# Kernel optimization log

Measured on AMD Instinct MI355X. Metric: run time of the kernel, lower is better.

Reference implementation:

```python
import jax, jax.numpy as jnp
import numpy as np

B, H, W, C, NH, K = 4, 56, 56, 128, 4, 7


def setup_inputs() -> dict:
    key = jax.random.key(0)
    ks = jax.random.split(key, 6)
    x = jax.random.normal(ks[0], (B, H, W, C), dtype=jnp.float32)
    w_qkv = jax.random.normal(ks[1], (C, 3 * C), dtype=jnp.float32) * 0.02
    b_qkv = jnp.zeros((3 * C,), dtype=jnp.float32)
    rpb = jax.random.normal(ks[2], (NH, 2 * K - 1, 2 * K - 1), dtype=jnp.float32) * 0.02
    w_proj = jax.random.normal(ks[3], (C, C), dtype=jnp.float32) * 0.02
    b_proj = jnp.zeros((C,), dtype=jnp.float32)
    return {"x": x, "w_qkv": w_qkv, "b_qkv": b_qkv, "rpb": rpb,
            "w_proj": w_proj, "b_proj": b_proj}


def reference(x, w_qkv, b_qkv, rpb, w_proj, b_proj):
    B_, H_, W_, C_ = x.shape
    nh = rpb.shape[0]
    k = (rpb.shape[1] + 1) // 2          # kernel_size
    hd = C_ // nh                        # head_dim
    nb = k // 2                          # neighborhood radius
    scale = hd ** -0.5

    qkv = (x @ w_qkv + b_qkv).reshape(B_, H_, W_, 3, nh, hd)
    q = qkv[:, :, :, 0].transpose(0, 3, 1, 2, 4) * scale   # [B,nh,H,W,hd]
    kk = qkv[:, :, :, 1].transpose(0, 3, 1, 2, 4)          # [B,nh,H,W,hd]
    v = qkv[:, :, :, 2].transpose(0, 3, 1, 2, 4)           # [B,nh,H,W,hd]

    # NATTEN window start indices: window clamped to stay in-bounds (query shifts off-center at edges)
    si = jnp.clip(jnp.arange(H_) - nb, 0, H_ - k)          # [H]
    sj = jnp.clip(jnp.arange(W_) - nb, 0, W_ - k)          # [W]
    idx_i = si[:, None] + jnp.arange(k)                    # [H,k] absolute key rows
    idx_j = sj[:, None] + jnp.arange(k)                    # [W,k] absolute key cols

    # gather neighborhood keys/values: [B,nh,H,k,W,k,hd] (axes: b n i p j q d)
    k_win = kk[:, :, idx_i][:, :, :, :, idx_j]
    v_win = v[:, :, idx_i][:, :, :, :, idx_j]

    # relative position bias: index = key_pos - query_pos + (k-1)
    rel_i = idx_i - jnp.arange(H_)[:, None] + (k - 1)      # [H,k]
    rel_j = idx_j - jnp.arange(W_)[:, None] + (k - 1)      # [W,k]
    bias = rpb[:, rel_i][:, :, :, rel_j]                   # [nh,H,k,W,k]
    bias = bias.transpose(0, 1, 3, 2, 4)                   # [nh,H,W,k,k]

    attn = jnp.einsum('bnijd,bnipjqd->bnijpq', q, k_win) + bias[None]
    attn = jax.nn.softmax(attn.reshape(B_, nh, H_, W_, k * k), axis=-1)
    attn = attn.reshape(B_, nh, H_, W_, k, k)

    out = jnp.einsum('bnijpq,bnipjqd->bnijd', attn, v_win)  # [B,nh,H,W,hd]
    out = out.transpose(0, 2, 3, 1, 4).reshape(B_, H_, W_, C_)
    return out @ w_proj + b_proj
```

## Files before the change

kernel.cpp:

```cpp
#include <hip/hip_runtime.h>

#define BATCH 4
#define HH 56
#define WW 56
#define CC 128
#define NHD 4
#define HD 32
#define KS 7
#define NB 3
#define HWSZ (HH * WW)
#define RPBW 13
#define QKV_N 384
#define QKV_ELE ((size_t)BATCH * NHD * HWSZ * HD)

typedef unsigned short u16;
typedef unsigned int   u32;
typedef short bf16x8 __attribute__((ext_vector_type(8)));
typedef short bf16x4 __attribute__((ext_vector_type(4)));
typedef float f32x4  __attribute__((ext_vector_type(4)));

static __device__ __forceinline__ u32 f2bf(float f) {
    u32 u = __float_as_uint(f);
    return (u + 0x7FFFu + ((u >> 16) & 1u)) >> 16;
}
static __device__ __forceinline__ float bf2f(u32 h) { return __uint_as_float(h << 16); }

static __device__ __forceinline__ u32 cvtpk(float lo, float hi) {
    u32 d;
    asm("v_cvt_pk_bf16_f32 %0, %1, %2" : "=v"(d) : "v"(lo), "v"(hi));
    return d;
}
static __device__ __forceinline__ void split2(float a, float b, u32& h, u32& l) {
    h = cvtpk(a, b);
    l = cvtpk(a - __uint_as_float(h << 16), b - __uint_as_float(h & 0xffff0000u));
}

#if __has_builtin(__builtin_amdgcn_mfma_f32_16x16x16bf16_1k)
#define MFMA16(a, b, c) __builtin_amdgcn_mfma_f32_16x16x16bf16_1k(a, b, c, 0, 0, 0)
#else
static __device__ __forceinline__ f32x4 mfma16_asm(bf16x4 a, bf16x4 b, f32x4 c) {
    asm("v_mfma_f32_16x16x16_bf16 %0, %1, %2, %0" : "+v"(c) : "v"(a), "v"(b));
    return c;
}
#define MFMA16(a, b, c) mfma16_asm(a, b, c)
#endif

__global__ __launch_bounds__(256) void prep_w(
    const float* __restrict__ w_qkv, const float* __restrict__ w_proj,
    u16* __restrict__ wqT_h, u16* __restrict__ wqT_l,
    u16* __restrict__ wpT_h, u16* __restrict__ wpT_l)
{
    const int e = blockIdx.x * 256 + threadIdx.x;
    float v; u16 *dh, *dl; int idx;
    if (e < 384 * 128) {
        const int n = e >> 7, k = e & 127;
        v = w_qkv[k * QKV_N + n];
        dh = wqT_h; dl = wqT_l; idx = e;
    } else {
        const int e2 = e - 384 * 128;
        const int n = e2 >> 7, k = e2 & 127;
        v = w_proj[k * CC + n];
        dh = wpT_h; dl = wpT_l; idx = e2;
    }
    const u32 h = f2bf(v);
    dh[idx] = (u16)h;
    dl[idx] = (u16)f2bf(v - bf2f(h));
}

#define LP 72

__global__ __launch_bounds__(256) void qkv_mfma(
    const float* __restrict__ x, const u16* __restrict__ wT_h,
    const u16* __restrict__ wT_l, const float* __restrict__ bias,
    float* __restrict__ qb, float* __restrict__ kb, float* __restrict__ vb)
{
    __shared__ __align__(16) u16 Ah[64 * LP], Al[64 * LP];
    __shared__ __align__(16) u16 Bh[128 * LP], Bl[128 * LP];

    const int tid  = threadIdx.x;
    const int lane = tid & 63;
    const int w    = tid >> 6;
    const int wr = w >> 1, wc = w & 1;
    const int lr = lane >> 4, lc = lane & 15;
    const int m0 = blockIdx.x * 64;
    const int tz = blockIdx.y;

    f32x4 acc[2][4];
    #pragma unroll
    for (int nt = 0; nt < 4; ++nt) {
        const float bn = bias[tz * 128 + wc * 64 + nt * 16 + lc];
        acc[0][nt] = (f32x4){bn, bn, bn, bn};
        acc[1][nt] = acc[0][nt];
    }

    for (int kc = 0; kc < 128; kc += 64) {
        #pragma unroll
        for (int it = 0; it < 4; ++it) {
            const int task = tid + it * 256;
            const int row = task >> 4, q4 = task & 15;
            const float4 xv = *(const float4*)(x + (size_t)(m0 + row) * CC + kc + 4 * q4);
            u32 h0, l0, h1, l1;
            split2(xv.x, xv.y, h0, l0);
            split2(xv.z, xv.w, h1, l1);
            const int off = row * LP + 4 * q4;
            *(uint2*)&Ah[off] = make_uint2(h0, h1);
            *(uint2*)&Al[off] = make_uint2(l0, l1);
        }
        #pragma unroll
        for (int it = 0; it < 8; ++it) {
            const int task = tid + it * 256;
            const int hl = task >> 10;
            const int t2 = task & 1023;
            const int n = t2 >> 3, q8 = t2 & 7;
            const u16* src = (hl ? wT_l : wT_h) + (size_t)(tz * 128 + n) * CC + kc + 8 * q8;
            const uint4 vv = *(const uint4*)src;
            u16* dst = (hl ? Bl : Bh) + n * LP + 8 * q8;
            *(uint4*)dst = vv;
        }
        __syncthreads();
        #pragma unroll
        for (int s = 0; s < 2; ++s) {
            const int ko = 32 * s + 8 * lr;
            bf16x8 bfh[4], bfl[4];
            #pragma unroll
            for (int nt = 0; nt < 4; ++nt) {
                const int bo = (wc * 64 + nt * 16 + lc) * LP + ko;
                bfh[nt] = *(const bf16x8*)&Bh[bo];
                bfl[nt] = *(const bf16x8*)&Bl[bo];
            }
            #pragma unroll
            for (int mt = 0; mt < 2; ++mt) {
                const int ao = (wr * 32 + mt * 16 + lc) * LP + ko;
                const bf16x8 afh = *(const bf16x8*)&Ah[ao];
                const bf16x8 afl = *(const bf16x8*)&Al[ao];
                #pragma unroll
                for (int nt = 0; nt < 4; ++nt) {
                    acc[mt][nt] = __builtin_amdgcn_mfma_f32_16x16x32_bf16(afh, bfh[nt], acc[mt][nt], 0, 0, 0);
                    acc[mt][nt] = __builtin_amdgcn_mfma_f32_16x16x32_bf16(afh, bfl[nt], acc[mt][nt], 0, 0, 0);
                    acc[mt][nt] = __builtin_amdgcn_mfma_f32_16x16x32_bf16(afl, bfh[nt], acc[mt][nt], 0, 0, 0);
                }
            }
        }
        __syncthreads();
    }

    const int tzz = tz;
    float* dst      = (tzz == 0) ? qb : (tzz == 1) ? kb : vb;
    const float scl = (tzz == 0) ? 0.17677669529663687f : 1.0f;
    const int b = m0 / HWSZ;
    #pragma unroll
    for (int mt = 0; mt < 2; ++mt) {
        #pragma unroll
        for (int nt = 0; nt < 4; ++nt) {
            const int n = wc * 64 + nt * 16 + lc;
            const int head = n >> 5, d = n & 31;
            #pragma unroll
            for (int r = 0; r < 4; ++r) {
                const int m  = m0 + wr * 32 + mt * 16 + lr * 4 + r;
                const int ij = m - b * HWSZ;
                dst[((size_t)(b * NHD + head) * HWSZ + ij) * HD + d] = acc[mt][nt][r] * scl;
            }
        }
    }
}

__global__ __launch_bounds__(256) void natten_attn(
    const float* __restrict__ qb, const float* __restrict__ kb,
    const float* __restrict__ vb, const float* __restrict__ rpb,
    float* __restrict__ ob)
{
    __shared__ __align__(16) u16 KhS[208 * 32];
    __shared__ __align__(16) u16 KlS[208 * 32];
    __shared__ __align__(16) u16 VhS[26 * 16 * 20];
    __shared__ __align__(16) u16 VlS[26 * 16 * 20];
    __shared__ float rpbs[RPBW * RPBW];

    const int tid  = threadIdx.x;
    const int lane = tid & 63;
    const int wv   = tid >> 6;
    const int g    = lane >> 4;
    const int cl   = lane & 15;

    const int ti = blockIdx.x / 7;
    const int tj = blockIdx.x % 7;
    const int head = blockIdx.y;
    const int b    = blockIdx.z;
    const int R0 = min(max(ti * 8 - NB, 0), HH - 14);
    const int C0 = min(max(tj * 8 - NB, 0), WW - 14);
    const size_t base = (size_t)(b * NHD + head) * HWSZ;

    const int qlq = 16 * wv + cl;
    const int qi  = ti * 8 + (qlq >> 3);
    const int qj  = tj * 8 + (qlq & 7);
    const float* qp = qb + (base + (size_t)qi * WW + qj) * HD + 8 * g;
    const float4 qv0 = *(const float4*)qp;
    const float4 qv1 = *(const float4*)(qp + 4);

    union U8 { u32 u[4]; bf16x8 v; };
    U8 uqh, uql;
    split2(qv0.x, qv0.y, uqh.u[0], uql.u[0]);
    split2(qv0.z, qv0.w, uqh.u[1], uql.u[1]);
    split2(qv1.x, qv1.y, uqh.u[2], uql.u[2]);
    split2(qv1.z, qv1.w, uqh.u[3], uql.u[3]);
    const bf16x8 Qh = uqh.v;
    const bf16x8 Ql = uql.v;

    if (tid < RPBW * RPBW) rpbs[tid] = rpb[head * (RPBW * RPBW) + tid];

    for (int idx = tid; idx < 1568; idx += 256) {
        const int pos = idx >> 3, c4 = idx & 7;
        const int ri = (pos * 293) >> 12;
        const int rj = pos - ri * 14;
        const float4 kv = *(const float4*)(kb + (base + (size_t)(R0 + ri) * WW + (C0 + rj)) * HD + 4 * c4);
        u32 h0, l0, h1, l1;
        split2(kv.x, kv.y, h0, l0);
        split2(kv.z, kv.w, h1, l1);
        *(uint2*)&KhS[pos * 32 + 4 * c4] = make_uint2(h0, h1);
        *(uint2*)&KlS[pos * 32 + 4 * c4] = make_uint2(l0, l1);
    }
    for (int idx = tid; idx < 784; idx += 256) {
        const int pr = idx >> 3, c4 = idx & 7;
        const int pos0 = 2 * pr;
        const int ri0 = (pos0 * 293) >> 12;       const int rj0 = pos0 - ri0 * 14;
        const int ri1 = ((pos0 + 1) * 293) >> 12; const int rj1 = pos0 + 1 - ri1 * 14;
        const float4 va = *(const float4*)(vb + (base + (size_t)(R0 + ri0) * WW + (C0 + rj0)) * HD + 4 * c4);
        const float4 vc = *(const float4*)(vb + (base + (size_t)(R0 + ri1) * WW + (C0 + rj1)) * HD + 4 * c4);
        const int t = pos0 >> 4, kk = pos0 & 15;
        const float a0[4] = {va.x, va.y, va.z, va.w};
        const float a1[4] = {vc.x, vc.y, vc.z, vc.w};
        #pragma unroll
        for (int i = 0; i < 4; ++i) {
            const int d = 4 * c4 + i;
            const int nt = d >> 4, cd = d & 15;
            u32 hh, ll;
            split2(a0[i], a1[i], hh, ll);
            const int off = ((nt * 13 + t) * 16 + cd) * 20 + kk;
            *(u32*)&VhS[off] = hh;
            *(u32*)&VlS[off] = ll;
        }
    }
    for (int idx = tid; idx < 384; idx += 256) {
        const int kp = idx % 6;
        int r = idx / 6;
        const int cd = r & 15; r >>= 4;
        const int nt = r & 1;  const int arr = r >> 1;
        u16* dst = arr ? VlS : VhS;
        *(u32*)&dst[((nt * 13 + 12) * 16 + cd) * 20 + 4 + 2 * kp] = 0u;
    }
    __syncthreads();

    const int qi0  = ti * 8 + 2 * wv;
    const int s_lo = min(max(qi0 - NB, 0), HH - KS);
    const int t0   = min(((s_lo - R0) * 14) >> 4, 5);

    f32x4 p[8];
    #pragma unroll
    for (int tt = 0; tt < 8; ++tt) p[tt] = (f32x4){0.f, 0.f, 0.f, 0.f};
    #pragma unroll
    for (int tt = 0; tt < 8; ++tt) {
        const int ro = (16 * (t0 + tt) + cl) * 32 + 8 * g;
        const bf16x8 kh = *(const bf16x8*)&KhS[ro];
        const bf16x8 kl = *(const bf16x8*)&KlS[ro];
        p[tt] = __builtin_amdgcn_mfma_f32_16x16x32_bf16(kh, Qh, p[tt], 0, 0, 0);
        p[tt] = __builtin_amdgcn_mfma_f32_16x16x32_bf16(kh, Ql, p[tt], 0, 0, 0);
        p[tt] = __builtin_amdgcn_mfma_f32_16x16x32_bf16(kl, Qh, p[tt], 0, 0, 0);
    }

    const int si = min(max(qi - NB, 0), HH - KS);
    const int sj = min(max(qj - NB, 0), WW - KS);
    const int r_si = si - R0, c_sj = sj - C0;
    const int aq = qi - R0, bq = qj - C0;

    float mmax = -3.0e38f;
    #pragma unroll
    for (int tt = 0; tt < 8; ++tt) {
        #pragma unroll
        for (int r = 0; r < 4; ++r) {
            const int pp = 16 * (t0 + tt) + 4 * g + r;
            const int rowp = (pp * 293) >> 12;
            const int colp = pp - rowp * 14;
            const bool ok = (pp < 196) && ((u32)(rowp - r_si) <= 6u) && ((u32)(colp - c_sj) <= 6u);
            int bidx = (rowp - aq + 6) * RPBW + (colp - bq + 6);
            bidx = ok ? bidx : 0;
            const float sv = ok ? (p[tt][r] + rpbs[bidx]) : -3.0e38f;
            p[tt][r] = sv;
            mmax = fmaxf(mmax, sv);
        }
    }
    mmax = fmaxf(mmax, __shfl_xor(mmax, 16, 64));
    mmax = fmaxf(mmax, __shfl_xor(mmax, 32, 64));

    float lsum = 0.f;
    #pragma unroll
    for (int tt = 0; tt < 8; ++tt) {
        #pragma unroll
        for (int r = 0; r < 4; ++r) {
            const float e = __expf(p[tt][r] - mmax);
            p[tt][r] = e;
            lsum += e;
        }
    }
    lsum += __shfl_xor(lsum, 16, 64);
    lsum += __shfl_xor(lsum, 32, 64);
    const float inv = 1.f / lsum;

    bf16x4 pah[8], pal[8];
    #pragma unroll
    for (int tt = 0; tt < 8; ++tt) {
        const float p0 = p[tt][0] * inv, p1 = p[tt][1] * inv;
        const float p2 = p[tt][2] * inv, p3 = p[tt][3] * inv;
        union U4 { u32 u[2]; bf16x4 v; } ua, ub;
        split2(p0, p1, ua.u[0], ub.u[0]);
        split2(p2, p3, ua.u[1], ub.u[1]);
        pah[tt] = ua.v;
        pal[tt] = ub.v;
    }

    f32x4 o[2];
    o[0] = (f32x4){0.f, 0.f, 0.f, 0.f};
    o[1] = (f32x4){0.f, 0.f, 0.f, 0.f};
    #pragma unroll
    for (int tt = 0; tt < 8; ++tt) {
        const int t = t0 + tt;
        #pragma unroll
        for (int nt = 0; nt < 2; ++nt) {
            const int off = ((nt * 13 + t) * 16 + cl) * 20 + 4 * g;
            const bf16x4 vh = *(const bf16x4*)&VhS[off];
            const bf16x4 vl = *(const bf16x4*)&VlS[off];
            o[nt] = MFMA16(pah[tt], vh, o[nt]);
            o[nt] = MFMA16(pal[tt], vh, o[nt]);
            o[nt] = MFMA16(pah[tt], vl, o[nt]);
        }
    }

    #pragma unroll
    for (int nt = 0; nt < 2; ++nt) {
        #pragma unroll
        for (int r = 0; r < 4; ++r) {
            const int qlo = 16 * wv + 4 * g + r;
            const int oqi = ti * 8 + (qlo >> 3);
            const int oqj = tj * 8 + (qlo & 7);
            ob[((size_t)b * HWSZ + (size_t)oqi * WW + oqj) * CC + head * HD + 16 * nt + cl] = o[nt][r];
        }
    }
}

__global__ __launch_bounds__(256) void proj_mfma(
    const float* __restrict__ a, const u16* __restrict__ wT_h,
    const u16* __restrict__ wT_l, const float* __restrict__ bias,
    float* __restrict__ out)
{
    __shared__ __align__(16) u16 Ah[32 * LP], Al[32 * LP];
    __shared__ __align__(16) u16 Bh[128 * LP], Bl[128 * LP];

    const int tid  = threadIdx.x;
    const int lane = tid & 63;
    const int w    = tid >> 6;
    const int wr = w >> 1, wc = w & 1;
    const int lr = lane >> 4, lc = lane & 15;
    const int m0 = blockIdx.x * 32;

    f32x4 acc[4];
    #pragma unroll
    for (int nt = 0; nt < 4; ++nt) {
        const float bn = bias[wc * 64 + nt * 16 + lc];
        acc[nt] = (f32x4){bn, bn, bn, bn};
    }

    for (int kc = 0; kc < 128; kc += 64) {
        #pragma unroll
        for (int it = 0; it < 2; ++it) {
            const int task = tid + it * 256;
            const int row = task >> 4, q4 = task & 15;
            const float4 xv = *(const float4*)(a + (size_t)(m0 + row) * CC + kc + 4 * q4);
            u32 h0, l0, h1, l1;
            split2(xv.x, xv.y, h0, l0);
            split2(xv.z, xv.w, h1, l1);
            const int off = row * LP + 4 * q4;
            *(uint2*)&Ah[off] = make_uint2(h0, h1);
            *(uint2*)&Al[off] = make_uint2(l0, l1);
        }
        #pragma unroll
        for (int it = 0; it < 8; ++it) {
            const int task = tid + it * 256;
            const int hl = task >> 10;
            const int t2 = task & 1023;
            const int n = t2 >> 3, q8 = t2 & 7;
            const u16* src = (hl ? wT_l : wT_h) + (size_t)n * CC + kc + 8 * q8;
            const uint4 vv = *(const uint4*)src;
            u16* dst = (hl ? Bl : Bh) + n * LP + 8 * q8;
            *(uint4*)dst = vv;
        }
        __syncthreads();
        #pragma unroll
        for (int s = 0; s < 2; ++s) {
            const int ko = 32 * s + 8 * lr;
            const int ao = (wr * 16 + lc) * LP + ko;
            const bf16x8 afh = *(const bf16x8*)&Ah[ao];
            const bf16x8 afl = *(const bf16x8*)&Al[ao];
            #pragma unroll
            for (int nt = 0; nt < 4; ++nt) {
                const int bo = (wc * 64 + nt * 16 + lc) * LP + ko;
                const bf16x8 bh = *(const bf16x8*)&Bh[bo];
                const bf16x8 bl = *(const bf16x8*)&Bl[bo];
                acc[nt] = __builtin_amdgcn_mfma_f32_16x16x32_bf16(afh, bh, acc[nt], 0, 0, 0);
                acc[nt] = __builtin_amdgcn_mfma_f32_16x16x32_bf16(afh, bl, acc[nt], 0, 0, 0);
                acc[nt] = __builtin_amdgcn_mfma_f32_16x16x32_bf16(afl, bh, acc[nt], 0, 0, 0);
            }
        }
        __syncthreads();
    }

    #pragma unroll
    for (int nt = 0; nt < 4; ++nt) {
        const int n = wc * 64 + nt * 16 + lc;
        #pragma unroll
        for (int r = 0; r < 4; ++r) {
            const int m = m0 + wr * 16 + lr * 4 + r;
            out[(size_t)m * CC + n] = acc[nt][r];
        }
    }
}

extern "C" void kernel_launch(void* const* d_in, const int* in_sizes, int n_in,
                              void* d_out, int out_size, void* d_ws, size_t ws_size,
                              hipStream_t stream) {
    const float* x      = (const float*)d_in[0];
    const float* w_qkv  = (const float*)d_in[1];
    const float* b_qkv  = (const float*)d_in[2];
    const float* rpb    = (const float*)d_in[3];
    const float* w_proj = (const float*)d_in[4];
    const float* b_proj = (const float*)d_in[5];
    float* out = (float*)d_out;

    float* ws  = (float*)d_ws;
    float* qbf = ws;
    float* kbf = ws + QKV_ELE;
    float* vbf = ws + 2 * QKV_ELE;
    float* obf = ws + 3 * QKV_ELE;
    u16* wqT_h = (u16*)(ws + 4 * QKV_ELE);
    u16* wqT_l = wqT_h + 384 * 128;
    u16* wpT_h = wqT_l + 384 * 128;
    u16* wpT_l = wpT_h + 128 * 128;

    prep_w<<<256, 256, 0, stream>>>(w_qkv, w_proj, wqT_h, wqT_l, wpT_h, wpT_l);
    qkv_mfma<<<dim3(196, 3), 256, 0, stream>>>(x, wqT_h, wqT_l, b_qkv, qbf, kbf, vbf);
    natten_attn<<<dim3(49, NHD, BATCH), 256, 0, stream>>>(qbf, kbf, vbf, rpb, obf);
    proj_mfma<<<392, 256, 0, stream>>>(obf, wpT_h, wpT_l, b_proj, out);
}
```

Baseline: 108.8 us.

## Fuse output projection into attention kernel via per-head atomic accumulation

Removes the separate projection kernel and the intermediate attention-output buffer. Each attention block now converts its 64x32 per-head output to split bf16, multiplies it by that head's slice of the projection weights with MFMA, and atomically adds the partial result into the final output. The output is pre-initialised with the projection bias inside the weight-prep kernel through extra blocks. This saves a global round trip and a launch, but adds float atomics from four heads per element (non-deterministic summation order) and extra LDS work in the attention kernel.

```diff
diff --git a/kernel.cpp b/kernel.cpp
--- a/kernel.cpp
+++ b/kernel.cpp
@@ -47,9 +47,17 @@
 
 __global__ __launch_bounds__(256) void prep_w(
     const float* __restrict__ w_qkv, const float* __restrict__ w_proj,
+    const float* __restrict__ b_proj,
     u16* __restrict__ wqT_h, u16* __restrict__ wqT_l,
-    u16* __restrict__ wpT_h, u16* __restrict__ wpT_l)
+    u16* __restrict__ wpT_h, u16* __restrict__ wpT_l,
+    float* __restrict__ out)
 {
+    if (blockIdx.x >= 256) {
+        const int idx = (blockIdx.x - 256) * 256 + threadIdx.x;
+        const int n4  = idx & 31;
+        ((float4*)out)[idx] = *(const float4*)(b_proj + 4 * n4);
+        return;
+    }
     const int e = blockIdx.x * 256 + threadIdx.x;
     float v; u16 *dh, *dl; int idx;
     if (e < 384 * 128) {
@@ -144,9 +152,8 @@
         __syncthreads();
     }
 
-    const int tzz = tz;
-    float* dst      = (tzz == 0) ? qb : (tzz == 1) ? kb : vb;
-    const float scl = (tzz == 0) ? 0.17677669529663687f : 1.0f;
+    float* dst      = (tz == 0) ? qb : (tz == 1) ? kb : vb;
+    const float scl = (tz == 0) ? 0.17677669529663687f : 1.0f;
     const int b = m0 / HWSZ;
     #pragma unroll
     for (int mt = 0; mt < 2; ++mt) {
@@ -167,13 +174,16 @@
 __global__ __launch_bounds__(256) void natten_attn(
     const float* __restrict__ qb, const float* __restrict__ kb,
     const float* __restrict__ vb, const float* __restrict__ rpb,
-    float* __restrict__ ob)
+    const u16* __restrict__ wpT_h, const u16* __restrict__ wpT_l,
+    float* __restrict__ outp)
 {
     __shared__ __align__(16) u16 KhS[208 * 32];
     __shared__ __align__(16) u16 KlS[208 * 32];
-    __shared__ __align__(16) u16 VhS[26 * 16 * 20];
-    __shared__ __align__(16) u16 VlS[26 * 16 * 20];
+    __shared__ __align__(16) u16 VBLOB[26 * 16 * 20 * 2];
     __shared__ float rpbs[RPBW * RPBW];
+
+    u16* const VhS = VBLOB;
+    u16* const VlS = VBLOB + 8320;
 
     const int tid  = threadIdx.x;
     const int lane = tid & 63;
@@ -333,91 +343,50 @@
         }
     }
 
+    __syncthreads();
+    u16* const Oh  = VBLOB;
+    u16* const Ol  = VBLOB + 2560;
+    u16* const Wph = VBLOB + 5120;
+    u16* const Wpl = VBLOB + 10240;
+
     #pragma unroll
     for (int nt = 0; nt < 2; ++nt) {
+        #pragma unroll
+        for (int r = 0; r < 4; ++r) {
+            const int q   = 16 * wv + 4 * g + r;
+            const float v = o[nt][r];
+            const u32 h   = f2bf(v);
+            const int off = q * 40 + 16 * nt + cl;
+            Oh[off] = (u16)h;
+            Ol[off] = (u16)f2bf(v - bf2f(h));
+        }
+    }
+    for (int idx = tid; idx < 1024; idx += 256) {
+        const int pl = idx >> 9;
+        const int t2 = idx & 511;
+        const int n = t2 >> 2, q8 = t2 & 3;
+        const u16* src = (pl ? wpT_l : wpT_h) + (size_t)n * CC + head * HD + 8 * q8;
+        u16* dst = (pl ? Wpl : Wph) + n * 40 + 8 * q8;
+        *(uint4*)dst = *(const uint4*)src;
+    }
+    __syncthreads();
+
+    const bf16x8 Afh = *(const bf16x8*)&Oh[(16 * wv + cl) * 40 + 8 * g];
+    const bf16x8 Afl = *(const bf16x8*)&Ol[(16 * wv + cl) * 40 + 8 * g];
+    #pragma unroll
+    for (int nt = 0; nt < 8; ++nt) {
+        const bf16x8 Bfh = *(const bf16x8*)&Wph[(16 * nt + cl) * 40 + 8 * g];
+        const bf16x8 Bfl = *(const bf16x8*)&Wpl[(16 * nt + cl) * 40 + 8 * g];
+        f32x4 c = (f32x4){0.f, 0.f, 0.f, 0.f};
+        c = __builtin_amdgcn_mfma_f32_16x16x32_bf16(Afh, Bfh, c, 0, 0, 0);
+        c = __builtin_amdgcn_mfma_f32_16x16x32_bf16(Afh, Bfl, c, 0, 0, 0);
+        c = __builtin_amdgcn_mfma_f32_16x16x32_bf16(Afl, Bfh, c, 0, 0, 0);
         #pragma unroll
         for (int r = 0; r < 4; ++r) {
             const int qlo = 16 * wv + 4 * g + r;
             const int oqi = ti * 8 + (qlo >> 3);
             const int oqj = tj * 8 + (qlo & 7);
-            ob[((size_t)b * HWSZ + (size_t)oqi * WW + oqj) * CC + head * HD + 16 * nt + cl] = o[nt][r];
-        }
-    }
-}
-
-__global__ __launch_bounds__(256) void proj_mfma(
-    const float* __restrict__ a, const u16* __restrict__ wT_h,
-    const u16* __restrict__ wT_l, const float* __restrict__ bias,
-    float* __restrict__ out)
-{
-    __shared__ __align__(16) u16 Ah[32 * LP], Al[32 * LP];
-    __shared__ __align__(16) u16 Bh[128 * LP], Bl[128 * LP];
-
-    const int tid  = threadIdx.x;
-    const int lane = tid & 63;
-    const int w    = tid >> 6;
-    const int wr = w >> 1, wc = w & 1;
-    const int lr = lane >> 4, lc = lane & 15;
-    const int m0 = blockIdx.x * 32;
-
-    f32x4 acc[4];
-    #pragma unroll
-    for (int nt = 0; nt < 4; ++nt) {
-        const float bn = bias[wc * 64 + nt * 16 + lc];
-        acc[nt] = (f32x4){bn, bn, bn, bn};
-    }
-
-    for (int kc = 0; kc < 128; kc += 64) {
-        #pragma unroll
-        for (int it = 0; it < 2; ++it) {
-            const int task = tid + it * 256;
-            const int row = task >> 4, q4 = task & 15;
-            const float4 xv = *(const float4*)(a + (size_t)(m0 + row) * CC + kc + 4 * q4);
-            u32 h0, l0, h1, l1;
-            split2(xv.x, xv.y, h0, l0);
-            split2(xv.z, xv.w, h1, l1);
-            const int off = row * LP + 4 * q4;
-            *(uint2*)&Ah[off] = make_uint2(h0, h1);
-            *(uint2*)&Al[off] = make_uint2(l0, l1);
-        }
-        #pragma unroll
-        for (int it = 0; it < 8; ++it) {
-            const int task = tid + it * 256;
-            const int hl = task >> 10;
-            const int t2 = task & 1023;
-            const int n = t2 >> 3, q8 = t2 & 7;
-            const u16* src = (hl ? wT_l : wT_h) + (size_t)n * CC + kc + 8 * q8;
-            const uint4 vv = *(const uint4*)src;
-            u16* dst = (hl ? Bl : Bh) + n * LP + 8 * q8;
-            *(uint4*)dst = vv;
-        }
-        __syncthreads();
-        #pragma unroll
-        for (int s = 0; s < 2; ++s) {
-            const int ko = 32 * s + 8 * lr;
-            const int ao = (wr * 16 + lc) * LP + ko;
-            const bf16x8 afh = *(const bf16x8*)&Ah[ao];
-            const bf16x8 afl = *(const bf16x8*)&Al[ao];
-            #pragma unroll
-            for (int nt = 0; nt < 4; ++nt) {
-                const int bo = (wc * 64 + nt * 16 + lc) * LP + ko;
-                const bf16x8 bh = *(const bf16x8*)&Bh[bo];
-                const bf16x8 bl = *(const bf16x8*)&Bl[bo];
-                acc[nt] = __builtin_amdgcn_mfma_f32_16x16x32_bf16(afh, bh, acc[nt], 0, 0, 0);
-                acc[nt] = __builtin_amdgcn_mfma_f32_16x16x32_bf16(afh, bl, acc[nt], 0, 0, 0);
-                acc[nt] = __builtin_amdgcn_mfma_f32_16x16x32_bf16(afl, bh, acc[nt], 0, 0, 0);
-            }
-        }
-        __syncthreads();
-    }
-
-    #pragma unroll
-    for (int nt = 0; nt < 4; ++nt) {
-        const int n = wc * 64 + nt * 16 + lc;
-        #pragma unroll
-        for (int r = 0; r < 4; ++r) {
-            const int m = m0 + wr * 16 + lr * 4 + r;
-            out[(size_t)m * CC + n] = acc[nt][r];
+            unsafeAtomicAdd(outp + ((size_t)b * HWSZ + (size_t)oqi * WW + oqj) * CC + 16 * nt + cl, c[r]);
         }
     }
 }
@@ -437,14 +406,14 @@
     float* qbf = ws;
     float* kbf = ws + QKV_ELE;
     float* vbf = ws + 2 * QKV_ELE;
-    float* obf = ws + 3 * QKV_ELE;
-    u16* wqT_h = (u16*)(ws + 4 * QKV_ELE);
+    u16* wqT_h = (u16*)(ws + 3 * QKV_ELE);
     u16* wqT_l = wqT_h + 384 * 128;
     u16* wpT_h = wqT_l + 384 * 128;
     u16* wpT_l = wpT_h + 128 * 128;
 
-    prep_w<<<256, 256, 0, stream>>>(w_qkv, w_proj, wqT_h, wqT_l, wpT_h, wpT_l);
+    prep_w<<<1824, 256, 0, stream>>>(w_qkv, w_proj, b_proj,
+                                     wqT_h, wqT_l, wpT_h, wpT_l, out);
     qkv_mfma<<<dim3(196, 3), 256, 0, stream>>>(x, wqT_h, wqT_l, b_qkv, qbf, kbf, vbf);
-    natten_attn<<<dim3(49, NHD, BATCH), 256, 0, stream>>>(qbf, kbf, vbf, rpb, obf);
-    proj_mfma<<<392, 256, 0, stream>>>(obf, wpT_h, wpT_l, b_proj, out);
-}
+    natten_attn<<<dim3(49, NHD, BATCH), 256, 0, stream>>>(qbf, kbf, vbf, rpb,
+                                                          wpT_h, wpT_l, out);
+}
```

Result: slower. 119.8 us (+10.2%).
